# Kernel optimization log

Hardware: AMD Instinct MI355X
Metric: run time of the kernel (lower is better)

## Reference

```python
import jax, jax.numpy as jnp
import numpy as np

D_MODEL = 1024
N_HEAD = 16
D_K = D_MODEL // N_HEAD


def setup_inputs() -> dict:
    key = jax.random.key(0)
    ks = jax.random.split(key, 11)
    B, S = 4, 2048
    s = 1.0 / np.sqrt(D_MODEL)
    return {
        "q": jax.random.normal(ks[0], (B, S, D_MODEL), jnp.float32),
        "k": jax.random.normal(ks[1], (B, S, D_MODEL), jnp.float32),
        "v": jax.random.normal(ks[2], (B, S, D_MODEL), jnp.float32),
        "w_q": jax.random.normal(ks[3], (D_MODEL, D_MODEL), jnp.float32) * s,
        "b_q": jnp.zeros((D_MODEL,), jnp.float32),
        "w_k": jax.random.normal(ks[4], (D_MODEL, D_MODEL), jnp.float32) * s,
        "b_k": jnp.zeros((D_MODEL,), jnp.float32),
        "w_v": jax.random.normal(ks[5], (D_MODEL, D_MODEL), jnp.float32) * s,
        "b_v": jnp.zeros((D_MODEL,), jnp.float32),
        "w_o": jax.random.normal(ks[6], (D_MODEL, D_MODEL), jnp.float32) * s,
        "b_o": jnp.zeros((D_MODEL,), jnp.float32),
    }


def reference(q, k, v, w_q, b_q, w_k, b_k, w_v, b_v, w_o, b_o):
    B, S, _ = q.shape
    # projections (torch Linear: x @ W^T + b)
    qp = q @ w_q.T + b_q
    kp = k @ w_k.T + b_k
    vp = v @ w_v.T + b_v
    # split heads -> [B, H, S, d_k]
    qh = qp.reshape(B, S, N_HEAD, D_K).transpose(0, 2, 1, 3)
    kh = kp.reshape(B, S, N_HEAD, D_K).transpose(0, 2, 1, 3)
    vh = vp.reshape(B, S, N_HEAD, D_K).transpose(0, 2, 1, 3)
    # scaled dot-product attention
    scores = jnp.einsum("bhqd,bhkd->bhqk", qh, kh) / jnp.sqrt(jnp.float32(D_K)).astype(qh.dtype)
    attn = jax.nn.softmax(scores, axis=-1)
    out = jnp.einsum("bhqk,bhkd->bhqd", attn, vh)
    # merge heads -> [B, S, d_model]
    out = out.transpose(0, 2, 1, 3).reshape(B, S, D_MODEL)
    return out @ w_o.T + b_o
```

## Files before the change

### kernel.cpp

```cpp
#include <hip/hip_runtime.h>
#include <hip/hip_bf16.h>
#include <stdint.h>

#define D_MODEL 1024
#define SEQ     2048
#define NBATCH  4
#define NHEAD   16
#define MROWS   (NBATCH*SEQ)

typedef __attribute__((ext_vector_type(8))) short short8;
typedef __attribute__((ext_vector_type(4))) float floatx4;
typedef __attribute__((ext_vector_type(2))) unsigned int uint2v;

#if __has_builtin(__builtin_amdgcn_exp2f)
#define EXP2(x) __builtin_amdgcn_exp2f(x)
#else
#define EXP2(x) exp2f(x)
#endif

__device__ __forceinline__ unsigned short f2bf(float f) {
  unsigned int x;
  __builtin_memcpy(&x, &f, 4);
  x += 0x7fffu + ((x >> 16) & 1u);
  return (unsigned short)(x >> 16);
}

__device__ __forceinline__ unsigned int pk2(float a, float b) {
  __hip_bfloat162 h = __float22bfloat162_rn(make_float2(a, b));
  unsigned int u;
  __builtin_memcpy(&u, &h, 4);
  return u;
}

__device__ __forceinline__ void gl_lds16(const unsigned short* g, unsigned short* l) {
  __builtin_amdgcn_global_load_lds(
      (const __attribute__((address_space(1))) unsigned int*)g,
      (__attribute__((address_space(3))) unsigned int*)l, 16, 0, 0);
}

__global__ __launch_bounds__(256)
void cvt_all(const float* __restrict__ q, const float* __restrict__ k,
             const float* __restrict__ v, const float* __restrict__ wq,
             const float* __restrict__ wk, const float* __restrict__ wv,
             const float* __restrict__ wo,
             unsigned short* __restrict__ dq, unsigned short* __restrict__ dk,
             unsigned short* __restrict__ dv, unsigned short* __restrict__ dwq,
             unsigned short* __restrict__ dwk, unsigned short* __restrict__ dwv,
             unsigned short* __restrict__ dwo) {
  const unsigned QV4 = (MROWS * D_MODEL) / 4u;
  const unsigned WV4 = (D_MODEL * D_MODEL) / 4u;
  const unsigned total = 3u * QV4 + 4u * WV4;
  for (unsigned i = blockIdx.x * 256u + threadIdx.x; i < total;
       i += gridDim.x * 256u) {
    const float* s;
    unsigned short* d;
    unsigned off;
    if (i < 3u * QV4) {
      const unsigned t = i >> 21;
      off = i & (QV4 - 1u);
      s = (t == 0) ? q : (t == 1) ? k : v;
      d = (t == 0) ? dq : (t == 1) ? dk : dv;
    } else {
      const unsigned j = i - 3u * QV4;
      const unsigned t = j >> 18;
      off = j & (WV4 - 1u);
      s = (t == 0) ? wq : (t == 1) ? wk : (t == 2) ? wv : wo;
      d = (t == 0) ? dwq : (t == 1) ? dwk : (t == 2) ? dwv : dwo;
    }
    const floatx4 f = *(const floatx4*)(s + (size_t)off * 4);
    uint2v u;
    u.x = pk2(f[0], f[1]);
    u.y = pk2(f[2], f[3]);
    *(uint2v*)(d + (size_t)off * 4) = u;
  }
}

template <int OMODE>
__device__ __forceinline__ void gemm_body(const unsigned short* __restrict__ A,
                                          const unsigned short* __restrict__ W,
                                          const float* __restrict__ bias,
                                          void* __restrict__ Y_,
                                          int M, int N, int K, float scale,
                                          unsigned short* As, unsigned short* Bs) {
  const int tid  = threadIdx.x;
  const int lane = tid & 63;
  const int w    = tid >> 6;
  const int rho  = lane & 15;
  const int quad = lane >> 4;
  const int ntile = N >> 7;
  const int cpx = gridDim.x >> 3;
  const int wg  = (blockIdx.x & 7) * cpx + (blockIdx.x >> 3);
  const int bx = wg % ntile;
  const int by = wg / ntile;
  const int tm = by << 7, tn = bx << 7;
  const int wrow = (w >> 1) << 6;
  const int wcol = (w & 1) << 6;

  const int lrow = lane >> 3;
  const int g    = ((lane & 7) - lrow) & 7;
  const unsigned short* gA = A + (size_t)(tm + w * 32 + lrow) * K + g * 8;
  const unsigned short* gB = W + (size_t)(tn + w * 32 + lrow) * K + g * 8;

  floatx4 acc[4][4] = {};

#define GSTAGE(buf, kk)                                                        \
  _Pragma("unroll") for (int c = 0; c < 4; c++) {                              \
    gl_lds16(gA + (size_t)c * 8 * K + (kk), &As[(buf)*8192 + (w*256 + c*64)*8]); \
    gl_lds16(gB + (size_t)c * 8 * K + (kk), &Bs[(buf)*8192 + (w*256 + c*64)*8]); \
  }

  GSTAGE(0, 0);
  __syncthreads();

  for (int kk = 0; kk < K; kk += 64) {
    const int cur = (kk >> 6) & 1;
    if (kk + 64 < K) { GSTAGE(cur ^ 1, kk + 64); }
    const unsigned short* as = &As[cur * 8192];
    const unsigned short* bs = &Bs[cur * 8192];
#pragma unroll
    for (int h = 0; h < 2; h++) {
      const int kp = (quad + rho + h * 4) & 7;
      short8 af[4], bf4[4];
#pragma unroll
      for (int i = 0; i < 4; i++)
        af[i] = *(const short8*)&as[(wrow + i * 16 + rho) * 64 + kp * 8];
#pragma unroll
      for (int j = 0; j < 4; j++)
        bf4[j] = *(const short8*)&bs[(wcol + j * 16 + rho) * 64 + kp * 8];
#pragma unroll
      for (int i = 0; i < 4; i++)
#pragma unroll
        for (int j = 0; j < 4; j++)
          acc[i][j] = __builtin_amdgcn_mfma_f32_16x16x32_bf16(af[i], bf4[j],
                                                              acc[i][j], 0, 0, 0);
    }
    __syncthreads();
  }
#undef GSTAGE

  float bj[4];
#pragma unroll
  for (int j = 0; j < 4; j++) bj[j] = bias[tn + wcol + j * 16 + rho];
#pragma unroll
  for (int i = 0; i < 4; i++) {
    const int grow = tm + wrow + i * 16 + (quad << 2);
#pragma unroll
    for (int j = 0; j < 4; j++) {
      const int gcol = tn + wcol + j * 16 + rho;
#pragma unroll
      for (int r = 0; r < 4; r++) {
        const float val = (acc[i][j][r] + bj[j]) * scale;
        if (OMODE == 1)
          ((float*)Y_)[(size_t)(grow + r) * N + gcol] = val;
        else
          ((unsigned short*)Y_)[(size_t)(grow + r) * N + gcol] = f2bf(val);
      }
    }
  }
}

template <int OMODE>
__global__ __launch_bounds__(256, 2)
void gemm_one(const unsigned short* __restrict__ A,
              const unsigned short* __restrict__ W,
              const float* __restrict__ bias, void* __restrict__ Y_,
              int M, int N, int K, float scale) {
  __shared__ __attribute__((aligned(16))) unsigned short As[2 * 128 * 64];
  __shared__ __attribute__((aligned(16))) unsigned short Bs[2 * 128 * 64];
  gemm_body<OMODE>(A, W, bias, Y_, M, N, K, scale, As, Bs);
}

__global__ __launch_bounds__(256, 2)
void gemm_qkv(const unsigned short* __restrict__ qb, const unsigned short* __restrict__ wqb,
              const float* __restrict__ bq, unsigned short* __restrict__ Qp,
              const unsigned short* __restrict__ kb, const unsigned short* __restrict__ wkb,
              const float* __restrict__ bk, unsigned short* __restrict__ Kp,
              const unsigned short* __restrict__ vb, const unsigned short* __restrict__ wvb,
              const float* __restrict__ bv, unsigned short* __restrict__ Vp,
              float qscale) {
  __shared__ __attribute__((aligned(16))) unsigned short As[2 * 128 * 64];
  __shared__ __attribute__((aligned(16))) unsigned short Bs[2 * 128 * 64];
  const int y = blockIdx.y;
  const unsigned short* A = (y == 0) ? qb : (y == 1) ? kb : vb;
  const unsigned short* W = (y == 0) ? wqb : (y == 1) ? wkb : wvb;
  const float* bias       = (y == 0) ? bq : (y == 1) ? bk : bv;
  unsigned short* Y       = (y == 0) ? Qp : (y == 1) ? Kp : Vp;
  const float scale = (y == 0) ? qscale : 1.0f;
  gemm_body<0>(A, W, bias, Y, MROWS, D_MODEL, D_MODEL, scale, As, Bs);
}

__device__ __forceinline__ void attn_step(const unsigned short* __restrict__ ks,
                                          const unsigned short* __restrict__ vt,
                                          const short8 (&aq)[4][2],
                                          float (&lsum)[4], floatx4 (&oacc)[4][4],
                                          int rho, int quad, int kp0, int kp1) {
  floatx4 sc[4][4];
#pragma unroll
  for (int gk = 0; gk < 4; gk++) {
    const int key = gk*16 + rho;
    const short8 kf0 = *(const short8*)(ks + (key*8 + kp0)*8);
    const short8 kf1 = *(const short8*)(ks + (key*8 + kp1)*8);
#pragma unroll
    for (int u = 0; u < 4; u++) {
      floatx4 t = {0.f, 0.f, 0.f, 0.f};
      t = __builtin_amdgcn_mfma_f32_16x16x32_bf16(kf0, aq[u][0], t, 0, 0, 0);
      t = __builtin_amdgcn_mfma_f32_16x16x32_bf16(kf1, aq[u][1], t, 0, 0, 0);
      sc[u][gk] = t;
    }
  }
  short8 pa0[4], pa1[4];
#pragma unroll
  for (int u = 0; u < 4; u++) {
    float E[4][4];
#pragma unroll
    for (int gk = 0; gk < 4; gk++)
#pragma unroll
      for (int r = 0; r < 4; r++) E[gk][r] = EXP2(sc[u][gk][r]);
    float s01 = 0.f, s23 = 0.f;
#pragma unroll
    for (int r = 0; r < 4; r++) { s01 += E[0][r] + E[1][r]; s23 += E[2][r] + E[3][r]; }
    lsum[u] += s01 + s23;
    union { short8 s; unsigned int w4[4]; } a0, a1;
    a0.w4[0] = pk2(E[0][0], E[0][1]); a0.w4[1] = pk2(E[0][2], E[0][3]);
    a0.w4[2] = pk2(E[1][0], E[1][1]); a0.w4[3] = pk2(E[1][2], E[1][3]);
    a1.w4[0] = pk2(E[2][0], E[2][1]); a1.w4[1] = pk2(E[2][2], E[2][3]);
    a1.w4[2] = pk2(E[3][0], E[3][1]); a1.w4[3] = pk2(E[3][2], E[3][3]);
    pa0[u] = a0.s; pa1[u] = a1.s;
  }
  short8 bv0[4], bv1[4];
#pragma unroll
  for (int c = 0; c < 4; c++) {
    bv0[c] = *(const short8*)&vt[(c*16 + rho)*72 + quad*8];
    bv1[c] = *(const short8*)&vt[(c*16 + rho)*72 + 32 + quad*8];
  }
#pragma unroll
  for (int u = 0; u < 4; u++)
#pragma unroll
    for (int c = 0; c < 4; c++) {
      oacc[u][c] = __builtin_amdgcn_mfma_f32_16x16x32_bf16(pa0[u], bv0[c], oacc[u][c], 0, 0, 0);
      oacc[u][c] = __builtin_amdgcn_mfma_f32_16x16x32_bf16(pa1[u], bv1[c], oacc[u][c], 0, 0, 0);
    }
}

__global__ __launch_bounds__(256, 2)
void attn_fused(const unsigned short* __restrict__ Qp,
                const unsigned short* __restrict__ Kp,
                const unsigned short* __restrict__ Vp,
                unsigned short* __restrict__ AO) {
  __shared__ unsigned short Ks[2][64*64];
  __shared__ unsigned short Vt[2][64*72];

  const int tid  = threadIdx.x;
  const int w    = tid >> 6;
  const int lane = tid & 63;
  const int rho  = lane & 15;
  const int quad = lane >> 4;

  const int qt = blockIdx.x >> 6;
  const int bh = blockIdx.x & 63;
  const int b  = bh >> 4;
  const int h  = bh & 15;
  const size_t base = (size_t)b*SEQ*D_MODEL + h*64;
  const unsigned short* Qb = Qp + base;
  const unsigned short* Kb = Kp + base;
  const unsigned short* Vb = Vp + base;

  const int q0 = qt*256 + w*64;

  short8 aq[4][2];
#pragma unroll
  for (int u = 0; u < 4; u++) {
    const unsigned short* qr = Qb + (size_t)(q0 + u*16 + rho)*D_MODEL + quad*8;
    aq[u][0] = *(const short8*)qr;
    aq[u][1] = *(const short8*)(qr + 32);
  }

  float lsum[4] = {};
  floatx4 oacc[4][4] = {};

  const int vkap = ((lane >> 2) & 3) * 8 + ((lane >> 4) & 1) * 4 + (lane & 3)
                 + (lane >> 5) * 32;

  const int s0 = w*64 + lane;
  const int k0key = s0 >> 3, k0g = ((s0 & 7) - k0key) & 7;
  const int s1 = 256 + w*64 + lane;
  const int k1key = s1 >> 3, k1g = ((s1 & 7) - k1key) & 7;

  const int kp0 = (quad + rho) & 7;
  const int kp1 = (kp0 + 4) & 7;

#define VLOAD(v0r, v1r, kbase)                                                 \
  { const unsigned short* vr = Vb + (size_t)((kbase) + lane)*D_MODEL + w*16;   \
    v0r = *(const short8*)vr; v1r = *(const short8*)(vr + 8); }
#define VWRITE(buf, v0r, v1r)                                                  \
  { unsigned short* dst = &Vt[buf][w*16*72 + vkap];                            \
    _Pragma("unroll") for (int e = 0; e < 8; e++) dst[e*72] = (unsigned short)v0r[e]; \
    _Pragma("unroll") for (int e = 0; e < 8; e++) dst[(8+e)*72] = (unsigned short)v1r[e]; }
#define KSTAGE(buf, kbase)                                                     \
  { gl_lds16(Kb + (size_t)((kbase) + k0key)*D_MODEL + k0g*8, &Ks[buf][(w*64)*8]);      \
    gl_lds16(Kb + (size_t)((kbase) + k1key)*D_MODEL + k1g*8, &Ks[buf][(256 + w*64)*8]); }

  short8 vA0, vA1, vB0, vB1;
  VLOAD(vA0, vA1, 0);
  KSTAGE(0, 0);

  for (int kb = 0; kb < SEQ; kb += 128) {
    VWRITE(0, vA0, vA1);
    __syncthreads();
    VLOAD(vB0, vB1, kb + 64);
    KSTAGE(1, kb + 64);
    attn_step(&Ks[0][0], &Vt[0][0], aq, lsum, oacc, rho, quad, kp0, kp1);

    VWRITE(1, vB0, vB1);
    __syncthreads();
    if (kb + 128 < SEQ) {
      VLOAD(vA0, vA1, kb + 128);
      KSTAGE(0, kb + 128);
    }
    attn_step(&Ks[1][0], &Vt[1][0], aq, lsum, oacc, rho, quad, kp0, kp1);
  }
#undef VLOAD
#undef VWRITE
#undef KSTAGE

#pragma unroll
  for (int u = 0; u < 4; u++) {
    lsum[u] += __shfl_xor(lsum[u], 16);
    lsum[u] += __shfl_xor(lsum[u], 32);
  }

#pragma unroll
  for (int u = 0; u < 4; u++) {
    float inv[4];
#pragma unroll
    for (int r = 0; r < 4; r++)
      inv[r] = 1.0f / __shfl(lsum[u], quad * 4 + r, 64);
#pragma unroll
    for (int c = 0; c < 4; c++)
#pragma unroll
      for (int r = 0; r < 4; r++)
        AO[base + (size_t)(q0 + u*16 + (quad << 2) + r)*D_MODEL + c*16 + rho] =
            f2bf(oacc[u][c][r] * inv[r]);
  }
}

extern "C" void kernel_launch(void* const* d_in, const int* in_sizes, int n_in,
                              void* d_out, int out_size, void* d_ws, size_t ws_size,
                              hipStream_t stream) {
  const float* q  = (const float*)d_in[0];
  const float* k  = (const float*)d_in[1];
  const float* v  = (const float*)d_in[2];
  const float* wq = (const float*)d_in[3];
  const float* bq = (const float*)d_in[4];
  const float* wk = (const float*)d_in[5];
  const float* bk = (const float*)d_in[6];
  const float* wv = (const float*)d_in[7];
  const float* bv = (const float*)d_in[8];
  const float* wo = (const float*)d_in[9];
  const float* bo = (const float*)d_in[10];
  float* out = (float*)d_out;

  unsigned short* Qp  = (unsigned short*)d_ws;
  unsigned short* Kp  = Qp + (size_t)MROWS*D_MODEL;
  unsigned short* Vp  = Kp + (size_t)MROWS*D_MODEL;
  unsigned short* AO  = Vp + (size_t)MROWS*D_MODEL;
  unsigned short* qb  = AO + (size_t)MROWS*D_MODEL;
  unsigned short* kb  = qb + (size_t)MROWS*D_MODEL;
  unsigned short* vb  = kb + (size_t)MROWS*D_MODEL;
  unsigned short* wqb = vb + (size_t)MROWS*D_MODEL;
  unsigned short* wkb = wqb + (size_t)D_MODEL*D_MODEL;
  unsigned short* wvb = wkb + (size_t)D_MODEL*D_MODEL;
  unsigned short* wob = wvb + (size_t)D_MODEL*D_MODEL;

  const float qscale = 0.125f * 1.4426950408889634f;

  const dim3 blk(256);
  cvt_all<<<dim3(2048), blk, 0, stream>>>(q, k, v, wq, wk, wv, wo,
                                          qb, kb, vb, wqb, wkb, wvb, wob);

  gemm_qkv<<<dim3((D_MODEL/128) * (MROWS/128), 3), blk, 0, stream>>>(
      qb, wqb, bq, Qp, kb, wkb, bk, Kp, vb, wvb, bv, Vp, qscale);

  attn_fused<<<dim3(NBATCH*NHEAD*(SEQ/256)), blk, 0, stream>>>(Qp, Kp, Vp, AO);

  gemm_one<1><<<dim3((D_MODEL/128) * (MROWS/128)), blk, 0, stream>>>(
      AO, wob, bo, out, MROWS, D_MODEL, D_MODEL, 1.0f);
}
```

Before: 314.7 us.

## Use 4-stage K=32 LDS pipeline in GEMMs and MFMA priority hints in attention

```diff
diff --git a/kernel.cpp b/kernel.cpp
--- a/kernel.cpp
+++ b/kernel.cpp
@@ -96,45 +96,48 @@
   const int wrow = (w >> 1) << 6;
   const int wcol = (w & 1) << 6;
 
-  const int lrow = lane >> 3;
-  const int g    = ((lane & 7) - lrow) & 7;
+  const int lrow = lane >> 2;
+  const int g    = ((lane & 3) - lrow) & 3;
   const unsigned short* gA = A + (size_t)(tm + w * 32 + lrow) * K + g * 8;
   const unsigned short* gB = W + (size_t)(tn + w * 32 + lrow) * K + g * 8;
 
   floatx4 acc[4][4] = {};
 
-#define GSTAGE(buf, kk)                                                        \
-  _Pragma("unroll") for (int c = 0; c < 4; c++) {                              \
-    gl_lds16(gA + (size_t)c * 8 * K + (kk), &As[(buf)*8192 + (w*256 + c*64)*8]); \
-    gl_lds16(gB + (size_t)c * 8 * K + (kk), &Bs[(buf)*8192 + (w*256 + c*64)*8]); \
-  }
+#define GSTAGE(slot, kk)                                                       \
+  { gl_lds16(gA + (kk),                  &As[(slot)*4096 + (w*32)*32]);        \
+    gl_lds16(gA + 16*(size_t)K + (kk),   &As[(slot)*4096 + (w*32 + 16)*32]);   \
+    gl_lds16(gB + (kk),                  &Bs[(slot)*4096 + (w*32)*32]);        \
+    gl_lds16(gB + 16*(size_t)K + (kk),   &Bs[(slot)*4096 + (w*32 + 16)*32]); }
 
   GSTAGE(0, 0);
-  __syncthreads();
-
-  for (int kk = 0; kk < K; kk += 64) {
-    const int cur = (kk >> 6) & 1;
-    if (kk + 64 < K) { GSTAGE(cur ^ 1, kk + 64); }
-    const unsigned short* as = &As[cur * 8192];
-    const unsigned short* bs = &Bs[cur * 8192];
-#pragma unroll
-    for (int h = 0; h < 2; h++) {
-      const int kp = (quad + rho + h * 4) & 7;
-      short8 af[4], bf4[4];
-#pragma unroll
-      for (int i = 0; i < 4; i++)
-        af[i] = *(const short8*)&as[(wrow + i * 16 + rho) * 64 + kp * 8];
+  GSTAGE(1, 32);
+  GSTAGE(2, 64);
+
+  const int T = K >> 5;
+  const int kp = ((quad + rho) & 3) * 8;
+
+  for (int t = 0; t < T; ++t) {
+    if (t <= T - 3)      asm volatile("s_waitcnt vmcnt(8)" ::: "memory");
+    else if (t == T - 2) asm volatile("s_waitcnt vmcnt(4)" ::: "memory");
+    else                 asm volatile("s_waitcnt vmcnt(0)" ::: "memory");
+    __builtin_amdgcn_s_barrier();
+    if (t + 3 < T) { GSTAGE((t + 3) & 3, (t + 3) * 32); }
+
+    const unsigned short* as = &As[(t & 3) * 4096];
+    const unsigned short* bs = &Bs[(t & 3) * 4096];
+    short8 af[4], bf4[4];
+#pragma unroll
+    for (int i = 0; i < 4; i++)
+      af[i] = *(const short8*)&as[(wrow + i * 16 + rho) * 32 + kp];
+#pragma unroll
+    for (int j = 0; j < 4; j++)
+      bf4[j] = *(const short8*)&bs[(wcol + j * 16 + rho) * 32 + kp];
+#pragma unroll
+    for (int i = 0; i < 4; i++)
 #pragma unroll
       for (int j = 0; j < 4; j++)
-        bf4[j] = *(const short8*)&bs[(wcol + j * 16 + rho) * 64 + kp * 8];
-#pragma unroll
-      for (int i = 0; i < 4; i++)
-#pragma unroll
-        for (int j = 0; j < 4; j++)
-          acc[i][j] = __builtin_amdgcn_mfma_f32_16x16x32_bf16(af[i], bf4[j],
-                                                              acc[i][j], 0, 0, 0);
-    }
-    __syncthreads();
+        acc[i][j] = __builtin_amdgcn_mfma_f32_16x16x32_bf16(af[i], bf4[j],
+                                                            acc[i][j], 0, 0, 0);
   }
 #undef GSTAGE
 
@@ -165,8 +168,8 @@
               const unsigned short* __restrict__ W,
               const float* __restrict__ bias, void* __restrict__ Y_,
               int M, int N, int K, float scale) {
-  __shared__ __attribute__((aligned(16))) unsigned short As[2 * 128 * 64];
-  __shared__ __attribute__((aligned(16))) unsigned short Bs[2 * 128 * 64];
+  __shared__ __attribute__((aligned(16))) unsigned short As[4 * 128 * 32];
+  __shared__ __attribute__((aligned(16))) unsigned short Bs[4 * 128 * 32];
   gemm_body<OMODE>(A, W, bias, Y_, M, N, K, scale, As, Bs);
 }
 
@@ -178,8 +181,8 @@
               const unsigned short* __restrict__ vb, const unsigned short* __restrict__ wvb,
               const float* __restrict__ bv, unsigned short* __restrict__ Vp,
               float qscale) {
-  __shared__ __attribute__((aligned(16))) unsigned short As[2 * 128 * 64];
-  __shared__ __attribute__((aligned(16))) unsigned short Bs[2 * 128 * 64];
+  __shared__ __attribute__((aligned(16))) unsigned short As[4 * 128 * 32];
+  __shared__ __attribute__((aligned(16))) unsigned short Bs[4 * 128 * 32];
   const int y = blockIdx.y;
   const unsigned short* A = (y == 0) ? qb : (y == 1) ? kb : vb;
   const unsigned short* W = (y == 0) ? wqb : (y == 1) ? wkb : wvb;
@@ -195,6 +198,7 @@
                                           float (&lsum)[4], floatx4 (&oacc)[4][4],
                                           int rho, int quad, int kp0, int kp1) {
   floatx4 sc[4][4];
+  __builtin_amdgcn_s_setprio(1);
 #pragma unroll
   for (int gk = 0; gk < 4; gk++) {
     const int key = gk*16 + rho;
@@ -208,6 +212,7 @@
       sc[u][gk] = t;
     }
   }
+  __builtin_amdgcn_s_setprio(0);
   short8 pa0[4], pa1[4];
 #pragma unroll
   for (int u = 0; u < 4; u++) {
@@ -233,6 +238,7 @@
     bv0[c] = *(const short8*)&vt[(c*16 + rho)*72 + quad*8];
     bv1[c] = *(const short8*)&vt[(c*16 + rho)*72 + 32 + quad*8];
   }
+  __builtin_amdgcn_s_setprio(1);
 #pragma unroll
   for (int u = 0; u < 4; u++)
 #pragma unroll
@@ -240,6 +246,7 @@
       oacc[u][c] = __builtin_amdgcn_mfma_f32_16x16x32_bf16(pa0[u], bv0[c], oacc[u][c], 0, 0, 0);
       oacc[u][c] = __builtin_amdgcn_mfma_f32_16x16x32_bf16(pa1[u], bv1[c], oacc[u][c], 0, 0, 0);
     }
+  __builtin_amdgcn_s_setprio(0);
 }
 
 __global__ __launch_bounds__(256, 2)
```

After: 343.9 us. 9.3% more time.

## Use 512-thread blocks for GEMMs and attention, widen GEMM N tile to 256

Applied to the files above, without the earlier changes.

```diff
diff --git a/kernel.cpp b/kernel.cpp
--- a/kernel.cpp
+++ b/kernel.cpp
@@ -87,27 +87,29 @@
   const int w    = tid >> 6;
   const int rho  = lane & 15;
   const int quad = lane >> 4;
-  const int ntile = N >> 7;
+  const int ntile = N >> 8;
   const int cpx = gridDim.x >> 3;
   const int wg  = (blockIdx.x & 7) * cpx + (blockIdx.x >> 3);
   const int bx = wg % ntile;
   const int by = wg / ntile;
-  const int tm = by << 7, tn = bx << 7;
-  const int wrow = (w >> 1) << 6;
-  const int wcol = (w & 1) << 6;
+  const int tm = by << 7, tn = bx << 8;
+  const int wrow = (w >> 2) << 6;
+  const int wcol = (w & 3) << 6;
 
   const int lrow = lane >> 3;
   const int g    = ((lane & 7) - lrow) & 7;
-  const unsigned short* gA = A + (size_t)(tm + w * 32 + lrow) * K + g * 8;
+  const unsigned short* gA = A + (size_t)(tm + w * 16 + lrow) * K + g * 8;
   const unsigned short* gB = W + (size_t)(tn + w * 32 + lrow) * K + g * 8;
 
   floatx4 acc[4][4] = {};
 
 #define GSTAGE(buf, kk)                                                        \
-  _Pragma("unroll") for (int c = 0; c < 4; c++) {                              \
-    gl_lds16(gA + (size_t)c * 8 * K + (kk), &As[(buf)*8192 + (w*256 + c*64)*8]); \
-    gl_lds16(gB + (size_t)c * 8 * K + (kk), &Bs[(buf)*8192 + (w*256 + c*64)*8]); \
-  }
+  { gl_lds16(gA + (kk),                 &As[(buf)*8192  + (w*16)*64]);         \
+    gl_lds16(gA + 8*(size_t)K + (kk),   &As[(buf)*8192  + (w*16 + 8)*64]);     \
+    gl_lds16(gB + (kk),                 &Bs[(buf)*16384 + (w*32)*64]);         \
+    gl_lds16(gB + 8*(size_t)K + (kk),   &Bs[(buf)*16384 + (w*32 + 8)*64]);     \
+    gl_lds16(gB + 16*(size_t)K + (kk),  &Bs[(buf)*16384 + (w*32 + 16)*64]);    \
+    gl_lds16(gB + 24*(size_t)K + (kk),  &Bs[(buf)*16384 + (w*32 + 24)*64]); }
 
   GSTAGE(0, 0);
   __syncthreads();
@@ -116,7 +118,7 @@
     const int cur = (kk >> 6) & 1;
     if (kk + 64 < K) { GSTAGE(cur ^ 1, kk + 64); }
     const unsigned short* as = &As[cur * 8192];
-    const unsigned short* bs = &Bs[cur * 8192];
+    const unsigned short* bs = &Bs[cur * 16384];
 #pragma unroll
     for (int h = 0; h < 2; h++) {
       const int kp = (quad + rho + h * 4) & 7;
@@ -160,17 +162,17 @@
 }
 
 template <int OMODE>
-__global__ __launch_bounds__(256, 2)
+__global__ __launch_bounds__(512, 2)
 void gemm_one(const unsigned short* __restrict__ A,
               const unsigned short* __restrict__ W,
               const float* __restrict__ bias, void* __restrict__ Y_,
               int M, int N, int K, float scale) {
   __shared__ __attribute__((aligned(16))) unsigned short As[2 * 128 * 64];
-  __shared__ __attribute__((aligned(16))) unsigned short Bs[2 * 128 * 64];
+  __shared__ __attribute__((aligned(16))) unsigned short Bs[2 * 256 * 64];
   gemm_body<OMODE>(A, W, bias, Y_, M, N, K, scale, As, Bs);
 }
 
-__global__ __launch_bounds__(256, 2)
+__global__ __launch_bounds__(512, 2)
 void gemm_qkv(const unsigned short* __restrict__ qb, const unsigned short* __restrict__ wqb,
               const float* __restrict__ bq, unsigned short* __restrict__ Qp,
               const unsigned short* __restrict__ kb, const unsigned short* __restrict__ wkb,
@@ -179,7 +181,7 @@
               const float* __restrict__ bv, unsigned short* __restrict__ Vp,
               float qscale) {
   __shared__ __attribute__((aligned(16))) unsigned short As[2 * 128 * 64];
-  __shared__ __attribute__((aligned(16))) unsigned short Bs[2 * 128 * 64];
+  __shared__ __attribute__((aligned(16))) unsigned short Bs[2 * 256 * 64];
   const int y = blockIdx.y;
   const unsigned short* A = (y == 0) ? qb : (y == 1) ? kb : vb;
   const unsigned short* W = (y == 0) ? wqb : (y == 1) ? wkb : wvb;
@@ -191,26 +193,28 @@
 
 __device__ __forceinline__ void attn_step(const unsigned short* __restrict__ ks,
                                           const unsigned short* __restrict__ vt,
-                                          const short8 (&aq)[4][2],
-                                          float (&lsum)[4], floatx4 (&oacc)[4][4],
+                                          const short8 (&aq)[2][2],
+                                          float (&lsum)[2], floatx4 (&oacc)[2][4],
                                           int rho, int quad, int kp0, int kp1) {
-  floatx4 sc[4][4];
+  floatx4 sc[2][4];
+  __builtin_amdgcn_s_setprio(1);
 #pragma unroll
   for (int gk = 0; gk < 4; gk++) {
     const int key = gk*16 + rho;
     const short8 kf0 = *(const short8*)(ks + (key*8 + kp0)*8);
     const short8 kf1 = *(const short8*)(ks + (key*8 + kp1)*8);
 #pragma unroll
-    for (int u = 0; u < 4; u++) {
+    for (int u = 0; u < 2; u++) {
       floatx4 t = {0.f, 0.f, 0.f, 0.f};
       t = __builtin_amdgcn_mfma_f32_16x16x32_bf16(kf0, aq[u][0], t, 0, 0, 0);
       t = __builtin_amdgcn_mfma_f32_16x16x32_bf16(kf1, aq[u][1], t, 0, 0, 0);
       sc[u][gk] = t;
     }
   }
-  short8 pa0[4], pa1[4];
-#pragma unroll
-  for (int u = 0; u < 4; u++) {
+  __builtin_amdgcn_s_setprio(0);
+  short8 pa0[2], pa1[2];
+#pragma unroll
+  for (int u = 0; u < 2; u++) {
     float E[4][4];
 #pragma unroll
     for (int gk = 0; gk < 4; gk++)
@@ -233,16 +237,18 @@
     bv0[c] = *(const short8*)&vt[(c*16 + rho)*72 + quad*8];
     bv1[c] = *(const short8*)&vt[(c*16 + rho)*72 + 32 + quad*8];
   }
-#pragma unroll
-  for (int u = 0; u < 4; u++)
+  __builtin_amdgcn_s_setprio(1);
+#pragma unroll
+  for (int u = 0; u < 2; u++)
 #pragma unroll
     for (int c = 0; c < 4; c++) {
       oacc[u][c] = __builtin_amdgcn_mfma_f32_16x16x32_bf16(pa0[u], bv0[c], oacc[u][c], 0, 0, 0);
       oacc[u][c] = __builtin_amdgcn_mfma_f32_16x16x32_bf16(pa1[u], bv1[c], oacc[u][c], 0, 0, 0);
     }
-}
-
-__global__ __launch_bounds__(256, 2)
+  __builtin_amdgcn_s_setprio(0);
+}
+
+__global__ __launch_bounds__(512, 4)
 void attn_fused(const unsigned short* __restrict__ Qp,
                 const unsigned short* __restrict__ Kp,
                 const unsigned short* __restrict__ Vp,
@@ -265,56 +271,52 @@
   const unsigned short* Kb = Kp + base;
   const unsigned short* Vb = Vp + base;
 
-  const int q0 = qt*256 + w*64;
-
-  short8 aq[4][2];
-#pragma unroll
-  for (int u = 0; u < 4; u++) {
+  const int q0 = qt*256 + w*32;
+
+  short8 aq[2][2];
+#pragma unroll
+  for (int u = 0; u < 2; u++) {
     const unsigned short* qr = Qb + (size_t)(q0 + u*16 + rho)*D_MODEL + quad*8;
     aq[u][0] = *(const short8*)qr;
     aq[u][1] = *(const short8*)(qr + 32);
   }
 
-  float lsum[4] = {};
-  floatx4 oacc[4][4] = {};
+  float lsum[2] = {};
+  floatx4 oacc[2][4] = {};
 
   const int vkap = ((lane >> 2) & 3) * 8 + ((lane >> 4) & 1) * 4 + (lane & 3)
                  + (lane >> 5) * 32;
 
   const int s0 = w*64 + lane;
   const int k0key = s0 >> 3, k0g = ((s0 & 7) - k0key) & 7;
-  const int s1 = 256 + w*64 + lane;
-  const int k1key = s1 >> 3, k1g = ((s1 & 7) - k1key) & 7;
 
   const int kp0 = (quad + rho) & 7;
   const int kp1 = (kp0 + 4) & 7;
 
-#define VLOAD(v0r, v1r, kbase)                                                 \
-  { const unsigned short* vr = Vb + (size_t)((kbase) + lane)*D_MODEL + w*16;   \
-    v0r = *(const short8*)vr; v1r = *(const short8*)(vr + 8); }
-#define VWRITE(buf, v0r, v1r)                                                  \
-  { unsigned short* dst = &Vt[buf][w*16*72 + vkap];                            \
-    _Pragma("unroll") for (int e = 0; e < 8; e++) dst[e*72] = (unsigned short)v0r[e]; \
-    _Pragma("unroll") for (int e = 0; e < 8; e++) dst[(8+e)*72] = (unsigned short)v1r[e]; }
+#define VLOAD(v0r, kbase)                                                      \
+  { const unsigned short* vr = Vb + (size_t)((kbase) + lane)*D_MODEL + w*8;    \
+    v0r = *(const short8*)vr; }
+#define VWRITE(buf, v0r)                                                       \
+  { unsigned short* dst = &Vt[buf][(w*8)*72 + vkap];                           \
+    _Pragma("unroll") for (int e = 0; e < 8; e++) dst[e*72] = (unsigned short)v0r[e]; }
 #define KSTAGE(buf, kbase)                                                     \
-  { gl_lds16(Kb + (size_t)((kbase) + k0key)*D_MODEL + k0g*8, &Ks[buf][(w*64)*8]);      \
-    gl_lds16(Kb + (size_t)((kbase) + k1key)*D_MODEL + k1g*8, &Ks[buf][(256 + w*64)*8]); }
-
-  short8 vA0, vA1, vB0, vB1;
-  VLOAD(vA0, vA1, 0);
+  { gl_lds16(Kb + (size_t)((kbase) + k0key)*D_MODEL + k0g*8, &Ks[buf][(w*64)*8]); }
+
+  short8 vA0, vB0;
+  VLOAD(vA0, 0);
   KSTAGE(0, 0);
 
   for (int kb = 0; kb < SEQ; kb += 128) {
-    VWRITE(0, vA0, vA1);
+    VWRITE(0, vA0);
     __syncthreads();
-    VLOAD(vB0, vB1, kb + 64);
+    VLOAD(vB0, kb + 64);
     KSTAGE(1, kb + 64);
     attn_step(&Ks[0][0], &Vt[0][0], aq, lsum, oacc, rho, quad, kp0, kp1);
 
-    VWRITE(1, vB0, vB1);
+    VWRITE(1, vB0);
     __syncthreads();
     if (kb + 128 < SEQ) {
-      VLOAD(vA0, vA1, kb + 128);
+      VLOAD(vA0, kb + 128);
       KSTAGE(0, kb + 128);
     }
     attn_step(&Ks[1][0], &Vt[1][0], aq, lsum, oacc, rho, quad, kp0, kp1);
@@ -324,13 +326,13 @@
 #undef KSTAGE
 
 #pragma unroll
-  for (int u = 0; u < 4; u++) {
+  for (int u = 0; u < 2; u++) {
     lsum[u] += __shfl_xor(lsum[u], 16);
     lsum[u] += __shfl_xor(lsum[u], 32);
   }
 
 #pragma unroll
-  for (int u = 0; u < 4; u++) {
+  for (int u = 0; u < 2; u++) {
     float inv[4];
 #pragma unroll
     for (int r = 0; r < 4; r++)
@@ -374,15 +376,14 @@
 
   const float qscale = 0.125f * 1.4426950408889634f;
 
-  const dim3 blk(256);
-  cvt_all<<<dim3(2048), blk, 0, stream>>>(q, k, v, wq, wk, wv, wo,
-                                          qb, kb, vb, wqb, wkb, wvb, wob);
-
-  gemm_qkv<<<dim3((D_MODEL/128) * (MROWS/128), 3), blk, 0, stream>>>(
+  cvt_all<<<dim3(2048), dim3(256), 0, stream>>>(q, k, v, wq, wk, wv, wo,
+                                                qb, kb, vb, wqb, wkb, wvb, wob);
+
+  gemm_qkv<<<dim3(256, 3), dim3(512), 0, stream>>>(
       qb, wqb, bq, Qp, kb, wkb, bk, Kp, vb, wvb, bv, Vp, qscale);
 
-  attn_fused<<<dim3(NBATCH*NHEAD*(SEQ/256)), blk, 0, stream>>>(Qp, Kp, Vp, AO);
-
-  gemm_one<1><<<dim3((D_MODEL/128) * (MROWS/128)), blk, 0, stream>>>(
+  attn_fused<<<dim3(NBATCH*NHEAD*(SEQ/256)), dim3(512), 0, stream>>>(Qp, Kp, Vp, AO);
+
+  gemm_one<1><<<dim3(256), dim3(512), 0, stream>>>(
       AO, wob, bo, out, MROWS, D_MODEL, D_MODEL, 1.0f);
 }
```

Result: slower. 345.4 us (+9.8%).
